# Performance work log

Hardware: AMD Instinct MI355X
Metric: run time of the kernel (lower is better)

Reference implementation:

```python
import jax, jax.numpy as jnp
import numpy as np

NUM_EXPERTS = 8
TOP_K = 2
RANK = 16
LORA_ALPHA = 32
SCALING = LORA_ALPHA / RANK  # 2.0


def setup_inputs() -> dict:
    key = jax.random.key(0)
    ks = jax.random.split(key, 6)
    B, S, D_IN, D_OUT = 4, 2048, 4096, 4096
    x = jax.random.normal(ks[0], (B, S, D_IN), dtype=jnp.float32)
    W_base = jax.random.normal(ks[1], (D_OUT, D_IN), dtype=jnp.float32) * 0.02
    b_base = jax.random.normal(ks[2], (D_OUT,), dtype=jnp.float32) * 0.02
    W_router = jax.random.normal(ks[3], (NUM_EXPERTS, D_IN), dtype=jnp.float32) * 0.02
    A = jax.random.normal(ks[4], (NUM_EXPERTS, RANK, D_IN), dtype=jnp.float32) * 0.02
    Bm = jax.random.normal(ks[5], (D_OUT, RANK), dtype=jnp.float32) * 0.02
    Bm = jnp.broadcast_to(Bm, (NUM_EXPERTS, D_OUT, RANK)) * jnp.arange(1, NUM_EXPERTS + 1, dtype=jnp.float32)[:, None, None] * 0.2
    return {"x": x, "W_base": W_base, "b_base": b_base, "W_router": W_router, "A": A, "B": Bm}


def reference(x, W_base, b_base, W_router, A, B):
    bs, seq, d_in = x.shape
    T = bs * seq
    xf = x.reshape(T, d_in)  # flatten tokens, as in torch .view(-1, d_in)

    # base linear layer
    base = xf @ W_base.T + b_base  # [T, d_out]

    # local router: logits -> top-k -> softmax over selected weights
    logits = xf @ W_router.T                      # [T, E]
    rw, sel = jax.lax.top_k(logits, TOP_K)        # [T, K] each
    rw = jax.nn.softmax(rw, axis=-1)              # router_norm == 'softmax'

    # per-token per-expert combine weight (zero for unselected experts);
    # mathematically identical to gather-LoRA-scatter since top-k experts
    # per token are distinct.
    onehot = jax.nn.one_hot(sel, NUM_EXPERTS, dtype=rw.dtype)  # [T, K, E]
    w = jnp.einsum('tk,tke->te', rw, onehot)                   # [T, E]

    # LoRA: down-project to tiny rank, weight, then up-project; contract
    # expert+rank together to avoid a [T, E, d_out] intermediate.
    h = jnp.einsum('td,erd->ter', xf, A)          # [T, E, r] (small)
    lora = jnp.einsum('ter,te,eor->to', h, w, B) * SCALING  # [T, d_out]

    return (base + lora).reshape(bs, seq, -1)
```

## Files before the change

kernel.cpp:

```cpp
#include <hip/hip_runtime.h>
#include <hip/hip_bf16.h>
#include <stdint.h>

#define T_TOKENS 8192
#define DIN      4096
#define DOUT     4096
#define NE       8
#define RANK     16
#define KEXT     128
#define KTOT     4224
#define NT       66
#define SCALING  2.0f

typedef __attribute__((ext_vector_type(8))) short   short8;
typedef __attribute__((ext_vector_type(4))) float   float4v;

__device__ __forceinline__ unsigned short f2bf(float f) {
    union { float f; unsigned int u; } c; c.f = f;
    unsigned int u = c.u;
    u += 0x7FFFu + ((u >> 16) & 1u);
    return (unsigned short)(u >> 16);
}

#define GLD_LDS(g, l) __builtin_amdgcn_global_load_lds( \
    (const __attribute__((address_space(1))) void*)(g), \
    (__attribute__((address_space(3))) void*)(l), 16, 0, 0)

__global__ __launch_bounds__(256) void k_front(const float* __restrict__ x,
                                               const float* __restrict__ Wr,
                                               const float* __restrict__ Wb,
                                               const float* __restrict__ A,
                                               const float* __restrict__ Bm,
                                               unsigned short* __restrict__ xa,
                                               unsigned short* __restrict__ Wa,
                                               unsigned short* __restrict__ Acat,
                                               float* __restrict__ w8) {
    int b = blockIdx.x;
    int tid = threadIdx.x;

    if (b < 2048) {
        int l = tid & 63, w = tid >> 6;
        int t = b * 4 + w;
        const float4* x4 = (const float4*)x;
        const float4* Wr4 = (const float4*)Wr;
        unsigned short* xarow = xa + (size_t)t * KTOT;

        float racc[NE];
#pragma unroll
        for (int e = 0; e < NE; e++) racc[e] = 0.f;

#pragma unroll 4
        for (int ci = 0; ci < 16; ci++) {
            float4 xv = x4[(size_t)t * 1024 + ci * 64 + l];
            ushort4 p;
            p.x = f2bf(xv.x); p.y = f2bf(xv.y);
            p.z = f2bf(xv.z); p.w = f2bf(xv.w);
            *(ushort4*)(xarow + (ci * 64 + l) * 4) = p;
#pragma unroll
            for (int e = 0; e < NE; e++) {
                float4 wv = Wr4[e * 1024 + ci * 64 + l];
                racc[e] += xv.x * wv.x + xv.y * wv.y + xv.z * wv.z + xv.w * wv.w;
            }
        }
#pragma unroll
        for (int e = 0; e < NE; e++) {
            float v = racc[e];
#pragma unroll
            for (int off = 32; off > 0; off >>= 1) v += __shfl_xor(v, off);
            racc[e] = v;
        }
        if (l == 0) {
            int e0 = 0;
#pragma unroll
            for (int e = 1; e < NE; e++) if (racc[e] > racc[e0]) e0 = e;
            int e1 = -1;
#pragma unroll
            for (int e = 0; e < NE; e++)
                if (e != e0 && (e1 < 0 || racc[e] > racc[e1])) e1 = e;
            float a1 = __expf(racc[e1] - racc[e0]);
            float inv = 1.0f / (1.0f + a1);
            float* wrow = w8 + t * NE;
#pragma unroll
            for (int e = 0; e < NE; e++)
                wrow[e] = (e == e0) ? inv * SCALING : ((e == e1) ? a1 * inv * SCALING : 0.f);
        }
    } else if (b < 6144) {
        int base = (b - 2048) * 1024 + tid;
#pragma unroll
        for (int j = 0; j < 4; j++) {
            int idx = base + j * 256;
            float4 v = ((const float4*)Wb)[idx];
            int o  = idx >> 10;
            int kc = idx & 1023;
            ushort4 p;
            p.x = f2bf(v.x); p.y = f2bf(v.y); p.z = f2bf(v.z); p.w = f2bf(v.w);
            *(ushort4*)(Wa + (size_t)o * KTOT + kc * 4) = p;
        }
    } else {
        int idx = (b - 6144) * 256 + tid;
        if (idx < 131072) {
            float4 v = ((const float4*)A)[idx];
            ushort4 p;
            p.x = f2bf(v.x); p.y = f2bf(v.y); p.z = f2bf(v.z); p.w = f2bf(v.w);
            *(ushort4*)(Acat + (size_t)idx * 4) = p;
        } else {
            int j = idx - 131072;
            int o = j >> 5;
            int q = j & 31;
            int e = q >> 2;
            float4 v = ((const float4*)Bm)[(size_t)e * 16384 + o * 4 + (q & 3)];
            ushort4 p;
            p.x = f2bf(v.x); p.y = f2bf(v.y); p.z = f2bf(v.z); p.w = f2bf(v.w);
            *(ushort4*)(Wa + (size_t)o * KTOT + DIN + q * 4) = p;
        }
    }
}

#define STAGEH(kt, bb) do { \
    int k0_ = (kt) * 128; \
    _Pragma("unroll") \
    for (int it_ = 0; it_ < 2; it_++) { \
        int c_ = it_ * 256 + tid; \
        int row_ = c_ >> 4, s_ = c_ & 15; \
        int kc_ = s_ ^ (row_ & 15); \
        GLD_LDS(xa + (size_t)(m0 + row_) * KTOT + k0_ + kc_ * 8, lds_x + (bb) * 4096 + c_ * 8); \
    } \
    _Pragma("unroll") \
    for (int it_ = 0; it_ < 8; it_++) { \
        int c_ = it_ * 256 + tid; \
        int row_ = c_ >> 4, s_ = c_ & 15; \
        int kc_ = s_ ^ (row_ & 15); \
        GLD_LDS(Acat + (size_t)row_ * DIN + k0_ + kc_ * 8, lds_a + (bb) * 16384 + c_ * 8); \
    } \
} while (0)

__global__ __launch_bounds__(256) void k_h(unsigned short* __restrict__ xa,
                                           const unsigned short* __restrict__ Acat,
                                           const float* __restrict__ w8) {
    __shared__ unsigned short lds_x[2 * 32 * 128];
    __shared__ unsigned short lds_a[2 * 128 * 128];
    int m0  = blockIdx.x * 32;
    int tid = threadIdx.x;
    int l = tid & 63, w = tid >> 6;
    int quad = l >> 4, lr = l & 15;

    float4v acc[2][2] = {};

    STAGEH(0, 0);
    for (int kt = 0; kt < 32; ++kt) {
        int bb = kt & 1;
        if (kt + 1 < 32) {
            STAGEH(kt + 1, bb ^ 1);
            asm volatile("s_waitcnt vmcnt(10)" ::: "memory");
        } else {
            asm volatile("s_waitcnt vmcnt(0)" ::: "memory");
        }
        __syncthreads();
        const unsigned short* lx = lds_x + bb * 4096;
        const unsigned short* la = lds_a + bb * 16384;
#pragma unroll
        for (int kk = 0; kk < 4; kk++) {
            int kc = kk * 4 + quad;
            short8 a[2], bfr[2];
#pragma unroll
            for (int mi = 0; mi < 2; mi++) {
                int row = mi * 16 + lr;
                a[mi] = *(const short8*)&lx[row * 128 + ((kc ^ lr) * 8)];
            }
#pragma unroll
            for (int ni = 0; ni < 2; ni++) {
                int row = w * 32 + ni * 16 + lr;
                bfr[ni] = *(const short8*)&la[row * 128 + ((kc ^ lr) * 8)];
            }
#pragma unroll
            for (int mi = 0; mi < 2; mi++)
#pragma unroll
                for (int ni = 0; ni < 2; ni++)
                    acc[mi][ni] = __builtin_amdgcn_mfma_f32_16x16x32_bf16(a[mi], bfr[ni], acc[mi][ni], 0, 0, 0);
        }
        __syncthreads();
    }

#pragma unroll
    for (int mi = 0; mi < 2; mi++)
#pragma unroll
        for (int ni = 0; ni < 2; ni++) {
            int col = w * 32 + ni * 16 + lr;
            int e = col >> 4;
#pragma unroll
            for (int i = 0; i < 4; i++) {
                int t = m0 + mi * 16 + quad * 4 + i;
                float v = acc[mi][ni][i] * w8[t * NE + e];
                xa[(size_t)t * KTOT + DIN + col] = f2bf(v);
            }
        }
}

#define LOADA(dst, basep, mlo) { \
    _Pragma("unroll") for (int i_ = 0; i_ < 4; i_++) \
        dst[i_] = *(const short8*)((basep) + aoff + ((mlo) + i_) * 1024); }
#define LOADB(dst, basep) { \
    _Pragma("unroll") for (int i_ = 0; i_ < 4; i_++) \
        dst[i_] = *(const short8*)((basep) + boff + i_ * 1024); }
#define MFMA44(mlo) { \
    __builtin_amdgcn_s_setprio(1); \
    _Pragma("unroll") for (int i_ = 0; i_ < 4; i_++) \
    _Pragma("unroll") for (int j_ = 0; j_ < 4; j_++) \
        acc[(mlo) + i_][j_] = __builtin_amdgcn_mfma_f32_16x16x32_bf16(af[i_], bf[j_], acc[(mlo) + i_][j_], 0, 0, 0); \
    __builtin_amdgcn_s_setprio(0); }
#define STAGE(srcP, regbase, ts, kh, tb) do { \
    const unsigned short* s_ = (srcP) + (size_t)((ts) * 64 + (kh) * 32); \
    char* d_ = smem + (regbase) + (tb) * 32768 + (kh) * 16384 + tid16; \
    GLD_LDS(s_, d_); \
    GLD_LDS(s_ + (size_t)128 * KTOT, d_ + 8192); \
} while (0)
#define BAR() __builtin_amdgcn_s_barrier()
#define LGKM0() do { asm volatile("s_waitcnt lgkmcnt(0)" ::: "memory"); \
                     __builtin_amdgcn_sched_barrier(0); } while (0)

__global__ __launch_bounds__(512, 2) void k_main(const unsigned short* __restrict__ xa,
                                                 const unsigned short* __restrict__ Wa,
                                                 const float* __restrict__ bias,
                                                 float* __restrict__ out) {
    extern __shared__ char smem[];
    int tid = threadIdx.x;
    int l = tid & 63, w = tid >> 6;
    int lr = l & 15, quad = l >> 4;
    int wm = w >> 2, wn = w & 3;

    int bid = blockIdx.x;
    int wg  = (bid & 7) * 64 + (bid >> 3);
    int bm  = wg & 31, bn = wg >> 5;

    int laneoff = (lr * 4 + (quad ^ ((lr >> 1) & 3))) * 16;
    int aoff = wm * 8192 + laneoff;
    int boff = wn * 4096 + laneoff;

    int srow  = w * 16 + ((tid >> 2) & 15);
    int skq   = (tid & 3) ^ ((tid >> 3) & 3);
    int tid16 = tid * 16;
    const unsigned short* srcA = xa + (size_t)(bm * 256 + srow) * KTOT + skq * 8;
    const unsigned short* srcB = Wa + (size_t)(bn * 256 + srow) * KTOT + skq * 8;

    float4v acc[8][4] = {};
    short8 af[4], bf[4];

    STAGE(srcA, 0,     0, 0, 0);
    STAGE(srcB, 65536, 0, 0, 0);
    STAGE(srcA, 0,     0, 1, 0);
    STAGE(srcB, 65536, 0, 1, 0);
    STAGE(srcA, 0,     1, 0, 1);
    STAGE(srcB, 65536, 1, 0, 1);
    asm volatile("s_waitcnt vmcnt(4)" ::: "memory");
    BAR();

    for (int t = 0; t < NT; ++t) {
        int buf  = t & 1, nbuf = buf ^ 1;
        int ts1  = (t + 1 < NT) ? t + 1 : NT - 1;
        int ts2  = (t + 2 < NT) ? t + 2 : NT - 1;
        const char* pa = smem + buf * 32768;
        const char* pb = smem + 65536 + buf * 32768;

        LOADA(af, pa, 0);
        LOADB(bf, pb);
        STAGE(srcA, 0, ts1, 1, nbuf);
        BAR(); LGKM0();
        MFMA44(0);
        BAR();

        LOADA(af, pa, 4);
        STAGE(srcB, 65536, ts1, 1, nbuf);
        BAR(); LGKM0();
        MFMA44(4);
        BAR();

        LOADA(af, pa + 16384, 0);
        LOADB(bf, pb + 16384);
        STAGE(srcA, 0, ts2, 0, buf);
        BAR(); LGKM0();
        MFMA44(0);
        BAR();

        LOADA(af, pa + 16384, 4);
        STAGE(srcB, 65536, ts2, 0, buf);
        asm volatile("s_waitcnt vmcnt(4)" ::: "memory");
        BAR(); LGKM0();
        MFMA44(4);
        BAR();
    }

    int trow0 = bm * 256 + wm * 128;
    int ocol0 = bn * 256 + wn * 64;
#pragma unroll
    for (int ni = 0; ni < 4; ni++) {
        int o = ocol0 + ni * 16 + lr;
        float bb = bias[o];
#pragma unroll
        for (int mi = 0; mi < 8; mi++) {
#pragma unroll
            for (int i = 0; i < 4; i++) {
                int trow = trow0 + mi * 16 + quad * 4 + i;
                out[(size_t)trow * DOUT + o] = acc[mi][ni][i] + bb;
            }
        }
    }
}

extern "C" void kernel_launch(void* const* d_in, const int* in_sizes, int n_in,
                              void* d_out, int out_size, void* d_ws, size_t ws_size,
                              hipStream_t stream) {
    const float* x  = (const float*)d_in[0];
    const float* Wb = (const float*)d_in[1];
    const float* bb = (const float*)d_in[2];
    const float* Wr = (const float*)d_in[3];
    const float* A  = (const float*)d_in[4];
    const float* Bm = (const float*)d_in[5];
    float* out = (float*)d_out;

    char* ws = (char*)d_ws;
    unsigned short* xa   = (unsigned short*)(ws);
    unsigned short* Wa   = (unsigned short*)(ws + 69206016);
    unsigned short* Acat = (unsigned short*)(ws + 69206016 + 34603008);
    float*          w8   = (float*)(ws + 69206016 + 34603008 + 1048576);

    static bool attr_done = false;
    if (!attr_done) {
        hipFuncSetAttribute((const void*)k_main,
                            hipFuncAttributeMaxDynamicSharedMemorySize, 131072);
        attr_done = true;
    }

    k_front<<<dim3(7168),  dim3(256), 0, stream>>>(x, Wr, Wb, A, Bm, xa, Wa, Acat, w8);
    k_h    <<<dim3(256),   dim3(256), 0, stream>>>(xa, Acat, w8);
    k_main <<<dim3(512),   dim3(512), 131072, stream>>>(xa, Wa, bb, out);
}
```

Before: 592.2 us.

## Switch main GEMM to 32x32x16 MFMA with two-phase pipeline and new tile mapping

Result: slower. 609.0 us (+2.8%).

```diff
diff --git a/kernel.cpp b/kernel.cpp
--- a/kernel.cpp
+++ b/kernel.cpp
@@ -12,8 +12,9 @@
 #define NT       66
 #define SCALING  2.0f
 
-typedef __attribute__((ext_vector_type(8))) short   short8;
-typedef __attribute__((ext_vector_type(4))) float   float4v;
+typedef __attribute__((ext_vector_type(8)))  short  short8;
+typedef __attribute__((ext_vector_type(4)))  float  float4v;
+typedef __attribute__((ext_vector_type(16))) float  f32x16;
 
 __device__ __forceinline__ unsigned short f2bf(float f) {
     union { float f; unsigned int u; } c; c.f = f;
@@ -196,18 +197,24 @@
         }
 }
 
-#define LOADA(dst, basep, mlo) { \
-    _Pragma("unroll") for (int i_ = 0; i_ < 4; i_++) \
-        dst[i_] = *(const short8*)((basep) + aoff + ((mlo) + i_) * 1024); }
-#define LOADB(dst, basep) { \
-    _Pragma("unroll") for (int i_ = 0; i_ < 4; i_++) \
-        dst[i_] = *(const short8*)((basep) + boff + i_ * 1024); }
-#define MFMA44(mlo) { \
+#define READ_AB(h) do { \
+    const char* pa_ = smem + buf * 32768 + (h) * 16384; \
+    const char* pb_ = pa_ + 65536; \
+    _Pragma("unroll") for (int mi_ = 0; mi_ < 4; mi_++) { \
+        af[0][mi_] = *(const short8*)(pa_ + aoff0 + mi_ * 2048); \
+        af[1][mi_] = *(const short8*)(pa_ + (aoff0 ^ 32) + mi_ * 2048); } \
+    _Pragma("unroll") for (int ni_ = 0; ni_ < 2; ni_++) { \
+        bfr[0][ni_] = *(const short8*)(pb_ + boff0 + ni_ * 2048); \
+        bfr[1][ni_] = *(const short8*)(pb_ + (boff0 ^ 32) + ni_ * 2048); } \
+} while (0)
+#define MFMA_PHASE() do { \
     __builtin_amdgcn_s_setprio(1); \
-    _Pragma("unroll") for (int i_ = 0; i_ < 4; i_++) \
-    _Pragma("unroll") for (int j_ = 0; j_ < 4; j_++) \
-        acc[(mlo) + i_][j_] = __builtin_amdgcn_mfma_f32_16x16x32_bf16(af[i_], bf[j_], acc[(mlo) + i_][j_], 0, 0, 0); \
-    __builtin_amdgcn_s_setprio(0); }
+    _Pragma("unroll") for (int kq_ = 0; kq_ < 2; kq_++) \
+    _Pragma("unroll") for (int mi_ = 0; mi_ < 4; mi_++) \
+    _Pragma("unroll") for (int ni_ = 0; ni_ < 2; ni_++) \
+        acc[mi_][ni_] = __builtin_amdgcn_mfma_f32_32x32x16_bf16(af[kq_][mi_], bfr[kq_][ni_], acc[mi_][ni_], 0, 0, 0); \
+    __builtin_amdgcn_s_setprio(0); \
+} while (0)
 #define STAGE(srcP, regbase, ts, kh, tb) do { \
     const unsigned short* s_ = (srcP) + (size_t)((ts) * 64 + (kh) * 32); \
     char* d_ = smem + (regbase) + (tb) * 32768 + (kh) * 16384 + tid16; \
@@ -229,12 +236,15 @@
     int wm = w >> 2, wn = w & 3;
 
     int bid = blockIdx.x;
-    int wg  = (bid & 7) * 64 + (bid >> 3);
-    int bm  = wg & 31, bn = wg >> 5;
-
-    int laneoff = (lr * 4 + (quad ^ ((lr >> 1) & 3))) * 16;
-    int aoff = wm * 8192 + laneoff;
-    int boff = wn * 4096 + laneoff;
+    int xcd = bid & 7, idx = bid >> 3;
+    int bm  = (xcd & 3) * 8 + (idx & 7);
+    int bn  = (xcd >> 2) * 8 + (idx >> 3);
+
+    int q1 = quad & 1, hi = quad >> 1;
+    int gx = (lr >> 1) & 3;
+    int g0 = ((hi ^ gx) << 4);
+    int aoff0 = (wm * 8 + q1) * 1024 + lr * 64 + g0;
+    int boff0 = (wn * 4 + q1) * 1024 + lr * 64 + g0;
 
     int srow  = w * 16 + ((tid >> 2) & 15);
     int skq   = (tid & 3) ^ ((tid >> 3) & 3);
@@ -242,65 +252,52 @@
     const unsigned short* srcA = xa + (size_t)(bm * 256 + srow) * KTOT + skq * 8;
     const unsigned short* srcB = Wa + (size_t)(bn * 256 + srow) * KTOT + skq * 8;
 
-    float4v acc[8][4] = {};
-    short8 af[4], bf[4];
-
-    STAGE(srcA, 0,     0, 0, 0);
-    STAGE(srcB, 65536, 0, 0, 0);
-    STAGE(srcA, 0,     0, 1, 0);
-    STAGE(srcB, 65536, 0, 1, 0);
-    STAGE(srcA, 0,     1, 0, 1);
-    STAGE(srcB, 65536, 1, 0, 1);
-    asm volatile("s_waitcnt vmcnt(4)" ::: "memory");
+    f32x16 acc[4][2] = {};
+    short8 af[2][4], bfr[2][2];
+
+    STAGE(srcA, 0,     0, 0, 0); STAGE(srcB, 65536, 0, 0, 0);
+    STAGE(srcA, 0,     0, 1, 0); STAGE(srcB, 65536, 0, 1, 0);
+    STAGE(srcA, 0,     1, 0, 1); STAGE(srcB, 65536, 1, 0, 1);
+    asm volatile("s_waitcnt vmcnt(8)" ::: "memory");
     BAR();
 
     for (int t = 0; t < NT; ++t) {
         int buf  = t & 1, nbuf = buf ^ 1;
         int ts1  = (t + 1 < NT) ? t + 1 : NT - 1;
         int ts2  = (t + 2 < NT) ? t + 2 : NT - 1;
-        const char* pa = smem + buf * 32768;
-        const char* pb = smem + 65536 + buf * 32768;
-
-        LOADA(af, pa, 0);
-        LOADB(bf, pb);
-        STAGE(srcA, 0, ts1, 1, nbuf);
+
+        READ_AB(0);
+        STAGE(srcA, 0,     ts1, 1, nbuf);
+        STAGE(srcB, 65536, ts1, 1, nbuf);
+        asm volatile("s_waitcnt vmcnt(8)" ::: "memory");
         BAR(); LGKM0();
-        MFMA44(0);
+        MFMA_PHASE();
         BAR();
 
-        LOADA(af, pa, 4);
-        STAGE(srcB, 65536, ts1, 1, nbuf);
+        READ_AB(1);
+        STAGE(srcA, 0,     ts2, 0, buf);
+        STAGE(srcB, 65536, ts2, 0, buf);
+        asm volatile("s_waitcnt vmcnt(8)" ::: "memory");
         BAR(); LGKM0();
-        MFMA44(4);
+        MFMA_PHASE();
         BAR();
-
-        LOADA(af, pa + 16384, 0);
-        LOADB(bf, pb + 16384);
-        STAGE(srcA, 0, ts2, 0, buf);
-        BAR(); LGKM0();
-        MFMA44(0);
-        BAR();
-
-        LOADA(af, pa + 16384, 4);
-        STAGE(srcB, 65536, ts2, 0, buf);
-        asm volatile("s_waitcnt vmcnt(4)" ::: "memory");
-        BAR(); LGKM0();
-        MFMA44(4);
-        BAR();
-    }
-
+    }
+    asm volatile("s_waitcnt vmcnt(0)" ::: "memory");
+
+    int hi2 = l >> 5;
+    int n31 = l & 31;
     int trow0 = bm * 256 + wm * 128;
     int ocol0 = bn * 256 + wn * 64;
 #pragma unroll
-    for (int ni = 0; ni < 4; ni++) {
-        int o = ocol0 + ni * 16 + lr;
+    for (int ni = 0; ni < 2; ni++) {
+        int o = ocol0 + ni * 32 + n31;
         float bb = bias[o];
 #pragma unroll
-        for (int mi = 0; mi < 8; mi++) {
-#pragma unroll
-            for (int i = 0; i < 4; i++) {
-                int trow = trow0 + mi * 16 + quad * 4 + i;
-                out[(size_t)trow * DOUT + o] = acc[mi][ni][i] + bb;
+        for (int mi = 0; mi < 4; mi++) {
+#pragma unroll
+            for (int r = 0; r < 16; r++) {
+                int trow = trow0 + mi * 32 + (r & 3) + 8 * (r >> 2) + 4 * hi2;
+                out[(size_t)trow * DOUT + o] = acc[mi][ni][r] + bb;
             }
         }
     }
```
